# Kernel optimization log

Hardware: AMD Instinct MI355X
Metric: run time of the kernel (lower is better)

The kernel has to match this reference:

```python
import jax, jax.numpy as jnp
import numpy as np

B = 16384
D_IN = 1024
H = 1024


def setup_inputs() -> dict:
    key = jax.random.key(0)
    k1, k2, k3, k4, k5 = jax.random.split(key, 5)
    scale = 1.0 / np.sqrt(H)
    return {
        "input": jax.random.normal(k1, (B, D_IN), dtype=jnp.float32),
        "hx": jax.random.normal(k2, (B, H), dtype=jnp.float32),
        "weight_ih": jax.random.uniform(k3, (3, H, D_IN), dtype=jnp.float32, minval=-scale, maxval=scale),
        "weight_hh": jax.random.uniform(k4, (3, H, H), dtype=jnp.float32, minval=-scale, maxval=scale),
        "bias": jax.random.uniform(k5, (3, H), dtype=jnp.float32, minval=-scale, maxval=scale),
    }


def reference(input, hx, weight_ih, weight_hh, bias):
    # Batched form of the per-element loop: mv(W, v) per row == v @ W.T
    # gates_i[g] = input @ weight_ih[g].T ; gates_h[g] = h @ weight_hh[g].T
    gi = jnp.einsum("bd,ghd->gbh", input, weight_ih)   # [3, B, H]
    z = jax.nn.sigmoid(gi[0] + hx @ weight_hh[0].T + bias[0])
    r = jax.nn.sigmoid(gi[1] + hx @ weight_hh[1].T + bias[1])
    n = jax.nn.relu(gi[2] + (hx * r) @ weight_hh[2].T + bias[2])
    return (1.0 - z) * n + z * hx
```

## Files before the change

### kernel.cpp

```cpp
#include <hip/hip_runtime.h>


typedef __bf16 bf16x8 __attribute__((ext_vector_type(8)));
typedef float f32x4 __attribute__((ext_vector_type(4)));

#define B_ROWS 16384
#define LDA 3072
#define LDB 2048


__global__ __launch_bounds__(256) void pack_A(const float* __restrict__ inp,
                                              const float* __restrict__ hx,
                                              __bf16* __restrict__ A) {
  int t = blockIdx.x * 256 + threadIdx.x;
  int row = t >> 7;
  int col = (t & 127) << 3;
  const float4* pi = reinterpret_cast<const float4*>(inp + ((size_t)row << 10) + col);
  const float4* ph = reinterpret_cast<const float4*>(hx + ((size_t)row << 10) + col);
  float4 a0 = pi[0], a1 = pi[1];
  float4 b0 = ph[0], b1 = ph[1];
  bf16x8 oa, ob;
  oa[0] = (__bf16)a0.x; oa[1] = (__bf16)a0.y; oa[2] = (__bf16)a0.z; oa[3] = (__bf16)a0.w;
  oa[4] = (__bf16)a1.x; oa[5] = (__bf16)a1.y; oa[6] = (__bf16)a1.z; oa[7] = (__bf16)a1.w;
  ob[0] = (__bf16)b0.x; ob[1] = (__bf16)b0.y; ob[2] = (__bf16)b0.z; ob[3] = (__bf16)b0.w;
  ob[4] = (__bf16)b1.x; ob[5] = (__bf16)b1.y; ob[6] = (__bf16)b1.z; ob[7] = (__bf16)b1.w;
  *reinterpret_cast<bf16x8*>(A + (size_t)row * LDA + col) = oa;
  *reinterpret_cast<bf16x8*>(A + (size_t)row * LDA + 1024 + col) = ob;
}

__global__ __launch_bounds__(256) void pack_W(const float* __restrict__ wih,
                                              const float* __restrict__ whh,
                                              __bf16* __restrict__ Wc) {
  int t = blockIdx.x * 256 + threadIdx.x;
  int n = t >> 7;
  int col = (t & 127) << 3;
  const float4* pi = reinterpret_cast<const float4*>(wih + ((size_t)n << 10) + col);
  const float4* ph = reinterpret_cast<const float4*>(whh + ((size_t)n << 10) + col);
  float4 a0 = pi[0], a1 = pi[1];
  float4 b0 = ph[0], b1 = ph[1];
  bf16x8 oa, ob;
  oa[0] = (__bf16)a0.x; oa[1] = (__bf16)a0.y; oa[2] = (__bf16)a0.z; oa[3] = (__bf16)a0.w;
  oa[4] = (__bf16)a1.x; oa[5] = (__bf16)a1.y; oa[6] = (__bf16)a1.z; oa[7] = (__bf16)a1.w;
  ob[0] = (__bf16)b0.x; ob[1] = (__bf16)b0.y; ob[2] = (__bf16)b0.z; ob[3] = (__bf16)b0.w;
  ob[4] = (__bf16)b1.x; ob[5] = (__bf16)b1.y; ob[6] = (__bf16)b1.z; ob[7] = (__bf16)b1.w;
  *reinterpret_cast<bf16x8*>(Wc + (size_t)n * LDB + col) = oa;
  *reinterpret_cast<bf16x8*>(Wc + (size_t)n * LDB + 1024 + col) = ob;
}


template <int MODE>
__global__ __launch_bounds__(256) void gemm_fused(__bf16* A,
                                                  const __bf16* __restrict__ Wc,
                                                  const float* __restrict__ hx,
                                                  const float* __restrict__ bias,
                                                  __bf16* __restrict__ Zbuf,
                                                  float* __restrict__ out) {
  __shared__ __attribute__((aligned(16))) __bf16 As[128 * 64];
  __shared__ __attribute__((aligned(16))) __bf16 Bs[128 * 64];

  const int tid = threadIdx.x;
  const int row0 = blockIdx.x * 128;
  const int col0 = blockIdx.y * 128;

  const __bf16* Brow = Wc + (size_t)((MODE ? 2048 : 0) + col0) * LDB;

  f32x4 acc[4][4] = {};

  const int lane = tid & 63;
  const int wid = tid >> 6;
  const int wr = wid >> 1;
  const int wc = wid & 1;

  for (int k0 = 0; k0 < 2048; k0 += 64) {
    const int kA = (MODE == 1 && k0 >= 1024) ? k0 + 1024 : k0;
#pragma unroll
    for (int i = 0; i < 4; ++i) {
      int idx = i * 256 + tid;
      int r = idx >> 3;
      int c = idx & 7;
      int sc = c ^ (r & 7);
      const __bf16* g = A + (size_t)(row0 + r) * LDA + kA + sc * 8;
      __builtin_amdgcn_global_load_lds((const __attribute__((address_space(1))) void*)g,
                                       (__attribute__((address_space(3))) void*)(As + idx * 8),
                                       16, 0, 0);
    }
#pragma unroll
    for (int i = 0; i < 4; ++i) {
      int idx = i * 256 + tid;
      int r = idx >> 3;
      int c = idx & 7;
      int sc = c ^ (r & 7);
      const __bf16* g = Brow + (size_t)r * LDB + k0 + sc * 8;
      __builtin_amdgcn_global_load_lds((const __attribute__((address_space(1))) void*)g,
                                       (__attribute__((address_space(3))) void*)(Bs + idx * 8),
                                       16, 0, 0);
    }
    __syncthreads();

#pragma unroll
    for (int kk = 0; kk < 2; ++kk) {
      bf16x8 af[4], bfr[4];
#pragma unroll
      for (int m = 0; m < 4; ++m) {
        int r = wr * 64 + m * 16 + (lane & 15);
        int c = kk * 4 + (lane >> 4);
        af[m] = *reinterpret_cast<const bf16x8*>(As + r * 64 + (c ^ (r & 7)) * 8);
      }
#pragma unroll
      for (int n = 0; n < 4; ++n) {
        int r = wc * 64 + n * 16 + (lane & 15);
        int c = kk * 4 + (lane >> 4);
        bfr[n] = *reinterpret_cast<const bf16x8*>(Bs + r * 64 + (c ^ (r & 7)) * 8);
      }
#pragma unroll
      for (int m = 0; m < 4; ++m)
#pragma unroll
        for (int n = 0; n < 4; ++n)
          acc[m][n] = __builtin_amdgcn_mfma_f32_16x16x32_bf16(af[m], bfr[n], acc[m][n], 0, 0, 0);
    }
    __syncthreads();
  }

#pragma unroll
  for (int m = 0; m < 4; ++m) {
#pragma unroll
    for (int n = 0; n < 4; ++n) {
      int col = col0 + wc * 64 + n * 16 + (lane & 15);
      int rbase = row0 + wr * 64 + m * 16 + (lane >> 4) * 4;
      if (MODE == 0) {
        int gate = col >> 10;
        int h = col & 1023;
        float b = bias[gate * 1024 + h];
#pragma unroll
        for (int j = 0; j < 4; ++j) {
          int rg = rbase + j;
          float x = acc[m][n][j] + b;
          float s = 1.f / (1.f + __expf(-x));
          if (gate == 0) {
            Zbuf[(size_t)rg * 1024 + h] = (__bf16)s;
          } else {
            float hv = hx[(size_t)rg * 1024 + h];
            A[(size_t)rg * LDA + 2048 + h] = (__bf16)(hv * s);
          }
        }
      } else {
        int h = col;
        float b = bias[2048 + h];
#pragma unroll
        for (int j = 0; j < 4; ++j) {
          int rg = rbase + j;
          float np = fmaxf(acc[m][n][j] + b, 0.f);
          float z = (float)Zbuf[(size_t)rg * 1024 + h];
          float hv = hx[(size_t)rg * 1024 + h];
          out[(size_t)rg * 1024 + h] = (1.f - z) * np + z * hv;
        }
      }
    }
  }
}


extern "C" void kernel_launch(void* const* d_in, const int* in_sizes, int n_in,
                              void* d_out, int out_size, void* d_ws, size_t ws_size,
                              hipStream_t stream) {
  const float* inp  = (const float*)d_in[0];
  const float* hx   = (const float*)d_in[1];
  const float* wih  = (const float*)d_in[2];
  const float* whh  = (const float*)d_in[3];
  const float* bias = (const float*)d_in[4];
  float* out = (float*)d_out;

  char* ws = (char*)d_ws;
  __bf16* A  = (__bf16*)ws;
  __bf16* Wc = (__bf16*)(ws + 100663296);
  __bf16* Z  = (__bf16*)(ws + 100663296 + 12582912);

  pack_A<<<8192, 256, 0, stream>>>(inp, hx, A);
  pack_W<<<1536, 256, 0, stream>>>(wih, whh, Wc);

  dim3 g1(B_ROWS / 128, 2048 / 128);
  gemm_fused<0><<<g1, 256, 0, stream>>>(A, Wc, hx, bias, Z, out);

  dim3 g2(B_ROWS / 128, 1024 / 128);
  gemm_fused<1><<<g2, 256, 0, stream>>>(A, Wc, hx, bias, Z, out);
}
```

Before: 352.4 us.

## Rewrite fused GEMMs as 256x256 tiles with 8 waves and double-buffered LDS pipeline

Replaces the 128x128, 4-wave GEMM with a 256x256 tile kernel of 8 waves that double-buffers A and B halves in 128 KB of dynamic LDS. Global-to-LDS staging of the next K-step is interleaved with MFMA phases, with explicit vmcnt waits and barriers, and MFMA priority is raised via s_setprio. The aim is to hide load latency and raise arithmetic intensity per byte loaded. The cost is more barriers, higher register pressure from 8x4 accumulators, and fewer resident blocks per CU.

```diff
diff --git a/kernel.cpp b/kernel.cpp
--- a/kernel.cpp
+++ b/kernel.cpp
@@ -4,9 +4,9 @@
 typedef __bf16 bf16x8 __attribute__((ext_vector_type(8)));
 typedef float f32x4 __attribute__((ext_vector_type(4)));
 
-#define B_ROWS 16384
 #define LDA 3072
 #define LDB 2048
+#define HALF 8192
 
 
 __global__ __launch_bounds__(256) void pack_A(const float* __restrict__ inp,
@@ -48,85 +48,156 @@
 }
 
 
+__device__ __forceinline__ void stage_half(const __bf16* g0, size_t ldg, __bf16* lh, int tid) {
+#pragma unroll
+  for (int ld = 0; ld < 2; ++ld) {
+    int idx = ld * 512 + tid;
+    int r = idx >> 3;
+    int c = idx & 7;
+    int sc = c ^ (r & 7);
+    const __bf16* g = g0 + (size_t)r * ldg + sc * 8;
+    __builtin_amdgcn_global_load_lds((const __attribute__((address_space(1))) void*)g,
+                                     (__attribute__((address_space(3))) void*)(lh + idx * 8),
+                                     16, 0, 0);
+  }
+}
+
+__device__ __forceinline__ void ldA(const __bf16* sAh, int p, int lane, bf16x8 (&af)[2][2]) {
+#pragma unroll
+  for (int m = 0; m < 2; ++m)
+#pragma unroll
+    for (int kk = 0; kk < 2; ++kk) {
+      int rr = p * 32 + m * 16 + (lane & 15);
+      int c = kk * 4 + (lane >> 4);
+      af[m][kk] = *reinterpret_cast<const bf16x8*>(sAh + (rr * 8 + (c ^ (rr & 7))) * 8);
+    }
+}
+
+__device__ __forceinline__ void ldB(const __bf16* sBh, int wcl, int lane, bf16x8 (&bfr)[4][2]) {
+#pragma unroll
+  for (int n = 0; n < 4; ++n)
+#pragma unroll
+    for (int kk = 0; kk < 2; ++kk) {
+      int rr = wcl + n * 16 + (lane & 15);
+      int c = kk * 4 + (lane >> 4);
+      bfr[n][kk] = *reinterpret_cast<const bf16x8*>(sBh + (rr * 8 + (c ^ (rr & 7))) * 8);
+    }
+}
+
+__device__ __forceinline__ void mfma16(const bf16x8 (&af)[2][2], const bf16x8 (&bfr)[4][2],
+                                       f32x4 (&acc)[8][4], int p) {
+  __builtin_amdgcn_s_setprio(1);
+#pragma unroll
+  for (int m = 0; m < 2; ++m)
+#pragma unroll
+    for (int n = 0; n < 4; ++n)
+#pragma unroll
+      for (int kk = 0; kk < 2; ++kk)
+        acc[p * 2 + m][n] =
+            __builtin_amdgcn_mfma_f32_16x16x32_bf16(af[m][kk], bfr[n][kk], acc[p * 2 + m][n], 0, 0, 0);
+  __builtin_amdgcn_s_setprio(0);
+}
+
+
 template <int MODE>
-__global__ __launch_bounds__(256) void gemm_fused(__bf16* A,
-                                                  const __bf16* __restrict__ Wc,
-                                                  const float* __restrict__ hx,
-                                                  const float* __restrict__ bias,
-                                                  __bf16* __restrict__ Zbuf,
-                                                  float* __restrict__ out) {
-  __shared__ __attribute__((aligned(16))) __bf16 As[128 * 64];
-  __shared__ __attribute__((aligned(16))) __bf16 Bs[128 * 64];
+__global__ __launch_bounds__(512, 2) void gemm8(__bf16* A, const __bf16* __restrict__ Wc,
+                                                const float* __restrict__ hx,
+                                                const float* __restrict__ bias,
+                                                __bf16* __restrict__ Zbuf,
+                                                float* __restrict__ out) {
+  extern __shared__ char smem[];
+  __bf16* sA = (__bf16*)smem;
+  __bf16* sB = (__bf16*)smem + 4 * HALF;
 
   const int tid = threadIdx.x;
-  const int row0 = blockIdx.x * 128;
-  const int col0 = blockIdx.y * 128;
-
-  const __bf16* Brow = Wc + (size_t)((MODE ? 2048 : 0) + col0) * LDB;
-
-  f32x4 acc[4][4] = {};
-
   const int lane = tid & 63;
   const int wid = tid >> 6;
-  const int wr = wid >> 1;
-  const int wc = wid & 1;
-
-  for (int k0 = 0; k0 < 2048; k0 += 64) {
-    const int kA = (MODE == 1 && k0 >= 1024) ? k0 + 1024 : k0;
-#pragma unroll
-    for (int i = 0; i < 4; ++i) {
-      int idx = i * 256 + tid;
-      int r = idx >> 3;
-      int c = idx & 7;
-      int sc = c ^ (r & 7);
-      const __bf16* g = A + (size_t)(row0 + r) * LDA + kA + sc * 8;
-      __builtin_amdgcn_global_load_lds((const __attribute__((address_space(1))) void*)g,
-                                       (__attribute__((address_space(3))) void*)(As + idx * 8),
-                                       16, 0, 0);
-    }
-#pragma unroll
-    for (int i = 0; i < 4; ++i) {
-      int idx = i * 256 + tid;
-      int r = idx >> 3;
-      int c = idx & 7;
-      int sc = c ^ (r & 7);
-      const __bf16* g = Brow + (size_t)r * LDB + k0 + sc * 8;
-      __builtin_amdgcn_global_load_lds((const __attribute__((address_space(1))) void*)g,
-                                       (__attribute__((address_space(3))) void*)(Bs + idx * 8),
-                                       16, 0, 0);
-    }
-    __syncthreads();
-
-#pragma unroll
-    for (int kk = 0; kk < 2; ++kk) {
-      bf16x8 af[4], bfr[4];
-#pragma unroll
-      for (int m = 0; m < 4; ++m) {
-        int r = wr * 64 + m * 16 + (lane & 15);
-        int c = kk * 4 + (lane >> 4);
-        af[m] = *reinterpret_cast<const bf16x8*>(As + r * 64 + (c ^ (r & 7)) * 8);
-      }
-#pragma unroll
-      for (int n = 0; n < 4; ++n) {
-        int r = wc * 64 + n * 16 + (lane & 15);
-        int c = kk * 4 + (lane >> 4);
-        bfr[n] = *reinterpret_cast<const bf16x8*>(Bs + r * 64 + (c ^ (r & 7)) * 8);
-      }
-#pragma unroll
-      for (int m = 0; m < 4; ++m)
-#pragma unroll
-        for (int n = 0; n < 4; ++n)
-          acc[m][n] = __builtin_amdgcn_mfma_f32_16x16x32_bf16(af[m], bfr[n], acc[m][n], 0, 0, 0);
-    }
-    __syncthreads();
+  const int wr = wid >> 2;
+  const int wc = wid & 3;
+  const int wcl = (wc & 1) * 64;
+
+  const int row0 = blockIdx.x * 256;
+  const int col0 = blockIdx.y * 256;
+
+  const __bf16* Abase = A + (size_t)row0 * LDA;
+  const __bf16* Bbase = Wc + (size_t)((MODE ? 2048 : 0) + col0) * LDB;
+
+  f32x4 acc[8][4] = {};
+
+  auto stageA = [&](int t, int h) {
+    int tw = t & 31;
+    int k = (MODE && tw >= 16) ? tw * 64 + 1024 : tw * 64;
+    stage_half(Abase + (size_t)(h * 128) * LDA + k, LDA, sA + (((t & 1) << 1) + h) * HALF, tid);
+  };
+  auto stageB = [&](int t, int h) {
+    int tw = t & 31;
+    stage_half(Bbase + (size_t)(h * 128) * LDB + tw * 64, LDB, sB + (((t & 1) << 1) + h) * HALF, tid);
+  };
+
+  const __bf16* sAE = sA + wr * HALF;
+  const __bf16* sAO = sA + (2 + wr) * HALF;
+  const __bf16* sBE = sB + (wc >> 1) * HALF;
+  const __bf16* sBO = sB + (2 + (wc >> 1)) * HALF;
+
+  stageA(0, 0); stageA(0, 1); stageB(0, 0); stageB(0, 1);
+  stageB(1, 0); stageB(1, 1);
+  asm volatile("s_waitcnt vmcnt(4)" ::: "memory");
+  __builtin_amdgcn_s_barrier();
+
+  for (int i = 0; i < 16; ++i) {
+    const int O = 2 * i + 1, EN = 2 * i + 2, ON = 2 * i + 3;
+    bf16x8 af[2][2], bfE[4][2], bfO[4][2];
+    ldA(sAE, 0, lane, af); ldB(sBE, wcl, lane, bfE);
+    stageA(O, 0);
+    __builtin_amdgcn_s_barrier();
+    mfma16(af, bfE, acc, 0);
+    __builtin_amdgcn_s_barrier();
+    ldA(sAE, 1, lane, af);
+    stageA(O, 1);
+    __builtin_amdgcn_s_barrier();
+    mfma16(af, bfE, acc, 1);
+    __builtin_amdgcn_s_barrier();
+    ldA(sAE, 2, lane, af);
+    stageB(EN, 0);
+    __builtin_amdgcn_s_barrier();
+    mfma16(af, bfE, acc, 2);
+    __builtin_amdgcn_s_barrier();
+    ldA(sAE, 3, lane, af);
+    stageB(EN, 1);
+    asm volatile("s_waitcnt vmcnt(4)" ::: "memory");
+    __builtin_amdgcn_s_barrier();
+    mfma16(af, bfE, acc, 3);
+    __builtin_amdgcn_s_barrier();
+    ldA(sAO, 0, lane, af); ldB(sBO, wcl, lane, bfO);
+    stageA(EN, 0);
+    __builtin_amdgcn_s_barrier();
+    mfma16(af, bfO, acc, 0);
+    __builtin_amdgcn_s_barrier();
+    ldA(sAO, 1, lane, af);
+    stageA(EN, 1);
+    __builtin_amdgcn_s_barrier();
+    mfma16(af, bfO, acc, 1);
+    __builtin_amdgcn_s_barrier();
+    ldA(sAO, 2, lane, af);
+    stageB(ON, 0);
+    __builtin_amdgcn_s_barrier();
+    mfma16(af, bfO, acc, 2);
+    __builtin_amdgcn_s_barrier();
+    ldA(sAO, 3, lane, af);
+    stageB(ON, 1);
+    asm volatile("s_waitcnt vmcnt(4)" ::: "memory");
+    __builtin_amdgcn_s_barrier();
+    mfma16(af, bfO, acc, 3);
+    __builtin_amdgcn_s_barrier();
   }
-
-#pragma unroll
-  for (int m = 0; m < 4; ++m) {
+  asm volatile("s_waitcnt vmcnt(0)" ::: "memory");
+
+#pragma unroll
+  for (int m = 0; m < 8; ++m) {
 #pragma unroll
     for (int n = 0; n < 4; ++n) {
       int col = col0 + wc * 64 + n * 16 + (lane & 15);
-      int rbase = row0 + wr * 64 + m * 16 + (lane >> 4) * 4;
+      int rbase = row0 + wr * 128 + m * 16 + (lane >> 4) * 4;
       if (MODE == 0) {
         int gate = col >> 10;
         int h = col & 1023;
@@ -144,15 +215,14 @@
           }
         }
       } else {
-        int h = col;
-        float b = bias[2048 + h];
+        float b = bias[2048 + col];
 #pragma unroll
         for (int j = 0; j < 4; ++j) {
           int rg = rbase + j;
           float np = fmaxf(acc[m][n][j] + b, 0.f);
-          float z = (float)Zbuf[(size_t)rg * 1024 + h];
-          float hv = hx[(size_t)rg * 1024 + h];
-          out[(size_t)rg * 1024 + h] = (1.f - z) * np + z * hv;
+          float z = (float)Zbuf[(size_t)rg * 1024 + col];
+          float hv = hx[(size_t)rg * 1024 + col];
+          out[(size_t)rg * 1024 + col] = (1.f - z) * np + z * hv;
         }
       }
     }
@@ -175,12 +245,15 @@
   __bf16* Wc = (__bf16*)(ws + 100663296);
   __bf16* Z  = (__bf16*)(ws + 100663296 + 12582912);
 
+  (void)hipFuncSetAttribute((const void*)gemm8<0>, hipFuncAttributeMaxDynamicSharedMemorySize, 131072);
+  (void)hipFuncSetAttribute((const void*)gemm8<1>, hipFuncAttributeMaxDynamicSharedMemorySize, 131072);
+
   pack_A<<<8192, 256, 0, stream>>>(inp, hx, A);
   pack_W<<<1536, 256, 0, stream>>>(wih, whh, Wc);
 
-  dim3 g1(B_ROWS / 128, 2048 / 128);
-  gemm_fused<0><<<g1, 256, 0, stream>>>(A, Wc, hx, bias, Z, out);
-
-  dim3 g2(B_ROWS / 128, 1024 / 128);
-  gemm_fused<1><<<g2, 256, 0, stream>>>(A, Wc, hx, bias, Z, out);
-}
+  dim3 g1(16384 / 256, 2048 / 256);
+  gemm8<0><<<g1, 512, 131072, stream>>>(A, Wc, hx, bias, Z, out);
+
+  dim3 g2(16384 / 256, 1024 / 256);
+  gemm8<1><<<g2, 512, 131072, stream>>>(A, Wc, hx, bias, Z, out);
+}
```

Measured after the change: 282.9 us. 19.7% less time.
